# Performance work log

Hardware: AMD Instinct MI355X
Metric: run time of the kernel (lower is better)

## Reference

```python
import jax, jax.numpy as jnp
import numpy as np

H = 512        # HIDDEN_SIZE
HEADS = 4      # MEM_HEAD
KDIM = 256     # K_DIM (= H//2), HEADS*KDIM == 2*H
HALF = KDIM // 2
KNN = 32
SUB = 512      # SUB_SIZE
MEM = SUB * SUB
BN_EPS = 1e-5


def setup_inputs() -> dict:
    key = jax.random.key(0)
    ks = jax.random.split(key, 6)
    x = jax.random.normal(ks[0], (32, 64, H), jnp.float32)
    w1 = jax.random.normal(ks[1], (H // 2, H), jnp.float32) / np.sqrt(H).astype(np.float32)
    b1 = jnp.zeros((H // 2,), jnp.float32)
    w2 = jax.random.normal(ks[2], (2 * H, H // 2), jnp.float32) / np.sqrt(H // 2).astype(np.float32)
    b2 = jnp.zeros((2 * H,), jnp.float32)
    bn_gamma = jnp.ones((KDIM,), jnp.float32)
    bn_beta = jnp.zeros((KDIM,), jnp.float32)
    keys = jax.random.normal(ks[3], (HEADS, 2, SUB, HALF), jnp.float32) / np.sqrt(HALF).astype(np.float32)
    values = jax.random.normal(ks[4], (MEM, H), jnp.float32) * (H ** -0.5)
    return dict(x=x, w1=w1, b1=b1, w2=w2, b2=b2,
                bn_gamma=bn_gamma, bn_beta=bn_beta, keys=keys, values=values)


def reference(x, w1, b1, w2, b2, bn_gamma, bn_beta, keys, values):
    B, L, _ = x.shape
    n = B * L
    # Query MLP: H -> H/2 -> 2H, viewed as (n, HEADS, KDIM)
    h = jax.nn.relu(jnp.einsum('blh,ch->blc', x, w1) + b1)
    q = jnp.einsum('blc,dc->bld', h, w2) + b2                      # (B, L, 2H)
    q = q.reshape(n, HEADS, KDIM)
    # BatchNorm1d over the K_DIM channel (training-mode batch stats)
    flat = q.reshape(-1, KDIM)
    mean = flat.mean(0)
    var = flat.var(0)
    q = (q - mean) * jax.lax.rsqrt(var + BN_EPS) * bn_gamma + bn_beta
    # Product-key double top-k
    q1, q2 = q[..., :HALF], q[..., HALF:]
    s1 = jnp.einsum('nhd,hkd->nhk', q1, keys[:, 0])                # (n, HEADS, SUB)
    s2 = jnp.einsum('nhd,hkd->nhk', q2, keys[:, 1])
    ts1, ti1 = jax.lax.top_k(s1, KNN)
    ts2, ti2 = jax.lax.top_k(s2, KNN)
    all_s = (ts1[..., :, None] + ts2[..., None, :]).reshape(n, HEADS, KNN * KNN)
    all_i = (ti1[..., :, None] * SUB + ti2[..., None, :]).reshape(n, HEADS, KNN * KNN)
    sc, best = jax.lax.top_k(all_s, KNN)                            # (n, HEADS, KNN)
    idx = jnp.take_along_axis(all_i, best, axis=-1)
    # Softmax over KNN within each head (scores viewed as (-1, KNN))
    w = jax.nn.softmax(sc, axis=-1)
    idx = idx.reshape(n, HEADS * KNN)
    w = w.reshape(n, HEADS * KNN)
    # EmbeddingBag(mode='sum') with per-sample weights
    out = jnp.einsum('nkh,nk->nh', values[idx], w)                  # (n, H)
    out = out.reshape(B, L, H)
    return out.sum(1)                                               # (B, H)
```

## Files before the change

### kernel.cpp

```cpp
#include <hip/hip_runtime.h>
#include <hip/hip_bf16.h>
#include <math.h>

#define N_TOK   2048
#define HDIM    512
#define HHALF   256
#define QDIM    1024
#define KDIM    256
#define HALF    128
#define HEADS   4
#define KNN     32
#define SUB     512
#define NROWS   8192

__device__ __forceinline__ void gemm_tile_nt(
    const float* __restrict__ A, int lda,
    const float* __restrict__ B, int ldb,
    float* __restrict__ C, int ldc,
    int K, const float* __restrict__ bias, bool relu,
    int m0, int n0)
{
    __shared__ float As[16][68];
    __shared__ float Bs[16][68];
    int tid = threadIdx.x;
    int tx = tid & 15;
    int ty = tid >> 4;
    int lr = tid >> 2;
    int lc = (tid & 3) * 4;

    float acc[4][4] = {};

    for (int k0 = 0; k0 < K; k0 += 16) {
        float4 a = *(const float4*)(A + (size_t)(m0 + lr) * lda + k0 + lc);
        float4 b = *(const float4*)(B + (size_t)(n0 + lr) * ldb + k0 + lc);
        As[lc + 0][lr] = a.x; As[lc + 1][lr] = a.y;
        As[lc + 2][lr] = a.z; As[lc + 3][lr] = a.w;
        Bs[lc + 0][lr] = b.x; Bs[lc + 1][lr] = b.y;
        Bs[lc + 2][lr] = b.z; Bs[lc + 3][lr] = b.w;
        __syncthreads();
#pragma unroll
        for (int k = 0; k < 16; ++k) {
            float4 av = *(const float4*)&As[k][ty * 4];
            float4 bv = *(const float4*)&Bs[k][tx * 4];
            acc[0][0] = fmaf(av.x, bv.x, acc[0][0]);
            acc[0][1] = fmaf(av.x, bv.y, acc[0][1]);
            acc[0][2] = fmaf(av.x, bv.z, acc[0][2]);
            acc[0][3] = fmaf(av.x, bv.w, acc[0][3]);
            acc[1][0] = fmaf(av.y, bv.x, acc[1][0]);
            acc[1][1] = fmaf(av.y, bv.y, acc[1][1]);
            acc[1][2] = fmaf(av.y, bv.z, acc[1][2]);
            acc[1][3] = fmaf(av.y, bv.w, acc[1][3]);
            acc[2][0] = fmaf(av.z, bv.x, acc[2][0]);
            acc[2][1] = fmaf(av.z, bv.y, acc[2][1]);
            acc[2][2] = fmaf(av.z, bv.z, acc[2][2]);
            acc[2][3] = fmaf(av.z, bv.w, acc[2][3]);
            acc[3][0] = fmaf(av.w, bv.x, acc[3][0]);
            acc[3][1] = fmaf(av.w, bv.y, acc[3][1]);
            acc[3][2] = fmaf(av.w, bv.z, acc[3][2]);
            acc[3][3] = fmaf(av.w, bv.w, acc[3][3]);
        }
        __syncthreads();
    }

    float4 bb = make_float4(0.f, 0.f, 0.f, 0.f);
    if (bias) {
        bb.x = bias[n0 + tx * 4 + 0];
        bb.y = bias[n0 + tx * 4 + 1];
        bb.z = bias[n0 + tx * 4 + 2];
        bb.w = bias[n0 + tx * 4 + 3];
    }
#pragma unroll
    for (int i = 0; i < 4; ++i) {
        int m = m0 + ty * 4 + i;
        float4 r;
        r.x = acc[i][0] + bb.x;
        r.y = acc[i][1] + bb.y;
        r.z = acc[i][2] + bb.z;
        r.w = acc[i][3] + bb.w;
        if (relu) {
            r.x = fmaxf(r.x, 0.f); r.y = fmaxf(r.y, 0.f);
            r.z = fmaxf(r.z, 0.f); r.w = fmaxf(r.w, 0.f);
        }
        *(float4*)(C + (size_t)m * ldc + n0 + tx * 4) = r;
    }
}

__global__ __launch_bounds__(256) void gemm_nt_kernel(
    const float* __restrict__ A, int lda,
    const float* __restrict__ B, int ldb,
    float* __restrict__ C, int ldc,
    int K, const float* __restrict__ bias, int relu)
{
    gemm_tile_nt(A, lda, B, ldb, C, ldc, K, bias, relu != 0,
                 blockIdx.x * 64, blockIdx.y * 64);
}

__global__ __launch_bounds__(256) void score_kernel(
    const float* __restrict__ q, const float* __restrict__ keys,
    float* __restrict__ s1, float* __restrict__ s2)
{
    int z = blockIdx.z;
    int hh = z >> 1;
    int half = z & 1;
    const float* A = q + hh * KDIM + half * HALF;
    const float* B = keys + (size_t)z * SUB * HALF;
    float* C = (half ? s2 : s1) + hh * SUB;
    gemm_tile_nt(A, QDIM, B, HALF, C, HEADS * SUB, HALF, nullptr, false,
                 blockIdx.x * 64, blockIdx.y * 64);
}

__global__ __launch_bounds__(256) void bnstat_kernel(
    const float* __restrict__ q, float* __restrict__ partial)
{
    int c = threadIdx.x;
    int b = blockIdx.x;
    const float* base = q + (size_t)b * 32 * KDIM;
    float s = 0.f, s2 = 0.f;
#pragma unroll 8
    for (int r = 0; r < 32; ++r) {
        float v = base[r * KDIM + c];
        s += v;
        s2 = fmaf(v, v, s2);
    }
    partial[b * KDIM + c] = s;
    partial[256 * KDIM + b * KDIM + c] = s2;
}

__global__ __launch_bounds__(256) void bnfinal_kernel(
    const float* __restrict__ partial,
    const float* __restrict__ gamma, const float* __restrict__ beta,
    float* __restrict__ scsh)
{
    int c = threadIdx.x;
    float s = 0.f, s2 = 0.f;
    for (int b = 0; b < 256; ++b) {
        s += partial[b * KDIM + c];
        s2 += partial[256 * KDIM + b * KDIM + c];
    }
    float mean = s * (1.f / (float)NROWS);
    float var = s2 * (1.f / (float)NROWS) - mean * mean;
    float rstd = rsqrtf(var + 1e-5f);
    float sc = rstd * gamma[c];
    scsh[c] = sc;
    scsh[KDIM + c] = beta[c] - mean * sc;
}

__global__ __launch_bounds__(256) void bnapply_kernel(
    float* __restrict__ q, const float* __restrict__ scsh)
{
    int c = threadIdx.x;
    float sc = scsh[c];
    float sh = scsh[KDIM + c];
    size_t base = (size_t)blockIdx.x * 1024 + c;
#pragma unroll
    for (int r = 0; r < 4; ++r) {
        float v = q[base + r * KDIM];
        q[base + r * KDIM] = fmaf(v, sc, sh);
    }
}

__device__ __forceinline__ unsigned fmap(float f) {
    unsigned u = __float_as_uint(f);
    return (u & 0x80000000u) ? ~u : (u | 0x80000000u);
}

__device__ __forceinline__ int mbcnt64(unsigned long long m) {
    return __builtin_amdgcn_mbcnt_hi((unsigned)(m >> 32),
           __builtin_amdgcn_mbcnt_lo((unsigned)(m & 0xffffffffu), 0));
}

__global__ __launch_bounds__(256) void topk_kernel(
    const float* __restrict__ s1, const float* __restrict__ s2,
    int* __restrict__ out_idx, float* __restrict__ out_w)
{
    int w = threadIdx.x >> 6;
    int lane = threadIdx.x & 63;
    int task = blockIdx.x * 4 + w;

    __shared__ float ts1[4][KNN]; __shared__ int ti1[4][KNN];
    __shared__ float ts2[4][KNN]; __shared__ int ti2[4][KNN];
    __shared__ float scv[4][KNN]; __shared__ int scp[4][KNN];

    for (int src = 0; src < 2; ++src) {
        const float* base = (src ? s2 : s1) + (size_t)task * SUB;
        float v[8]; unsigned u[8];
#pragma unroll
        for (int i = 0; i < 8; ++i) {
            v[i] = base[lane + 64 * i];
            u[i] = fmap(v[i]);
        }
        unsigned t = 0u;
        for (int bit = 31; bit >= 0; --bit) {
            unsigned cand = t | (1u << bit);
            int cnt = 0;
#pragma unroll
            for (int i = 0; i < 8; ++i)
                cnt += __popcll(__ballot(u[i] >= cand));
            if (cnt >= KNN) t = cand;
        }
        float* tsv = src ? ts2[w] : ts1[w];
        int*   tsi = src ? ti2[w] : ti1[w];
        int pbase = 0;
#pragma unroll
        for (int i = 0; i < 8; ++i) {
            unsigned long long m = __ballot(u[i] >= t);
            if (u[i] >= t) {
                int pos = pbase + mbcnt64(m);
                if (pos < KNN) { tsv[pos] = v[i]; tsi[pos] = lane + 64 * i; }
            }
            pbase += __popcll(m);
        }
    }
    __syncthreads();

    float cv[16]; unsigned cu[16];
#pragma unroll
    for (int i = 0; i < 16; ++i) {
        int p = lane + 64 * i;
        cv[i] = ts1[w][p >> 5] + ts2[w][p & 31];
        cu[i] = fmap(cv[i]);
    }
    unsigned t2 = 0u;
    for (int bit = 31; bit >= 0; --bit) {
        unsigned cand = t2 | (1u << bit);
        int cnt = 0;
#pragma unroll
        for (int i = 0; i < 16; ++i)
            cnt += __popcll(__ballot(cu[i] >= cand));
        if (cnt >= KNN) t2 = cand;
    }
    int pbase = 0;
#pragma unroll
    for (int i = 0; i < 16; ++i) {
        unsigned long long m = __ballot(cu[i] >= t2);
        if (cu[i] >= t2) {
            int pos = pbase + mbcnt64(m);
            if (pos < KNN) { scv[w][pos] = cv[i]; scp[w][pos] = lane + 64 * i; }
        }
        pbase += __popcll(m);
    }
    __syncthreads();

    float x = (lane < KNN) ? scv[w][lane] : -3.0e38f;
    float mx = x;
#pragma unroll
    for (int off = 32; off; off >>= 1) mx = fmaxf(mx, __shfl_xor(mx, off));
    float e = (lane < KNN) ? expf(x - mx) : 0.f;
    float ssum = e;
#pragma unroll
    for (int off = 32; off; off >>= 1) ssum += __shfl_xor(ssum, off);

    if (lane < KNN) {
        int p = scp[w][lane];
        int i = p >> 5, j = p & 31;
        int gidx = ti1[w][i] * SUB + ti2[w][j];
        int n = task >> 2, h = task & 3;
        out_idx[n * (HEADS * KNN) + h * KNN + lane] = gidx;
        out_w[n * (HEADS * KNN) + h * KNN + lane] = e / ssum;
    }
}

__global__ __launch_bounds__(256) void gather_kernel(
    const float* __restrict__ values, const int* __restrict__ idx,
    const float* __restrict__ w, float* __restrict__ rows)
{
    int n = blockIdx.x;
    int tid = threadIdx.x;
    int pair = tid >> 7;
    int c4 = tid & 127;
    __shared__ int sidx[HEADS * KNN];
    __shared__ float sw[HEADS * KNN];
    __shared__ float4 tmp[128];
    if (tid < HEADS * KNN) {
        sidx[tid] = idx[n * (HEADS * KNN) + tid];
        sw[tid] = w[n * (HEADS * KNN) + tid];
    }
    __syncthreads();
    const float4* vv = (const float4*)values;
    float4 acc = make_float4(0.f, 0.f, 0.f, 0.f);
#pragma unroll 8
    for (int k = pair; k < HEADS * KNN; k += 2) {
        float4 v = vv[(size_t)sidx[k] * (HDIM / 4) + c4];
        float wk = sw[k];
        acc.x = fmaf(wk, v.x, acc.x);
        acc.y = fmaf(wk, v.y, acc.y);
        acc.z = fmaf(wk, v.z, acc.z);
        acc.w = fmaf(wk, v.w, acc.w);
    }
    if (pair) tmp[c4] = acc;
    __syncthreads();
    if (!pair) {
        float4 o = tmp[c4];
        acc.x += o.x; acc.y += o.y; acc.z += o.z; acc.w += o.w;
        ((float4*)rows)[(size_t)n * (HDIM / 4) + c4] = acc;
    }
}

__global__ __launch_bounds__(512) void reduce_kernel(
    const float* __restrict__ rows, float* __restrict__ out)
{
    int b = blockIdx.x;
    int c = threadIdx.x;
    float s = 0.f;
    for (int l = 0; l < 64; ++l)
        s += rows[(size_t)(b * 64 + l) * HDIM + c];
    out[b * HDIM + c] = s;
}

extern "C" void kernel_launch(void* const* d_in, const int* in_sizes, int n_in,
                              void* d_out, int out_size, void* d_ws, size_t ws_size,
                              hipStream_t stream)
{
    const float* x      = (const float*)d_in[0];
    const float* w1     = (const float*)d_in[1];
    const float* b1     = (const float*)d_in[2];
    const float* w2     = (const float*)d_in[3];
    const float* b2     = (const float*)d_in[4];
    const float* gamma  = (const float*)d_in[5];
    const float* beta   = (const float*)d_in[6];
    const float* keys   = (const float*)d_in[7];
    const float* values = (const float*)d_in[8];
    float* out = (float*)d_out;

    float* ws = (float*)d_ws;
    float* h       = ws;
    float* q       = h + N_TOK * HHALF;
    float* partial = q + N_TOK * QDIM;
    float* scsh    = partial + 2 * 256 * KDIM;
    float* s1      = scsh + 2 * KDIM;
    float* s2      = s1 + (size_t)N_TOK * HEADS * SUB;
    int*   tidx    = (int*)(s2 + (size_t)N_TOK * HEADS * SUB);
    float* tw      = (float*)(tidx + N_TOK * HEADS * KNN);
    float* rows    = tw + N_TOK * HEADS * KNN;

    gemm_nt_kernel<<<dim3(N_TOK / 64, HHALF / 64), 256, 0, stream>>>(
        x, HDIM, w1, HDIM, h, HHALF, HDIM, b1, 1);

    gemm_nt_kernel<<<dim3(N_TOK / 64, QDIM / 64), 256, 0, stream>>>(
        h, HHALF, w2, HHALF, q, QDIM, HHALF, b2, 0);

    bnstat_kernel<<<256, 256, 0, stream>>>(q, partial);
    bnfinal_kernel<<<1, 256, 0, stream>>>(partial, gamma, beta, scsh);
    bnapply_kernel<<<N_TOK, 256, 0, stream>>>(q, scsh);

    score_kernel<<<dim3(N_TOK / 64, SUB / 64, HEADS * 2), 256, 0, stream>>>(
        q, keys, s1, s2);

    topk_kernel<<<N_TOK * HEADS / 4, 256, 0, stream>>>(s1, s2, tidx, tw);

    gather_kernel<<<N_TOK, 256, 0, stream>>>(values, tidx, tw, rows);

    reduce_kernel<<<32, 512, 0, stream>>>(rows, out);
}
```

Baseline: 796.5 us.

## Fuse BN stats into fc2 GEMM, fold BN into keys, enlarge score tiles

Batch-norm statistics are now accumulated in the epilogue of the second MLP GEMM, which removes the separate stats pass over q. The normalization is no longer applied to q; it is folded algebraically into the product keys (keys scaled per channel, shift turned into a per-key bias), which removes the apply pass. The score GEMM moves to 128x128 tiles with 8x8 register blocking for more reuse. The top-k radix threshold search also exits early once exactly KNN candidates remain. The trade-off is higher register pressure in the score kernel and slightly different float rounding from the folded normalization.

After: 772.9 us. 3.0% less time.

```diff
diff --git a/kernel.cpp b/kernel.cpp
--- a/kernel.cpp
+++ b/kernel.cpp
@@ -95,47 +95,108 @@
                  blockIdx.x * 64, blockIdx.y * 64);
 }
 
-__global__ __launch_bounds__(256) void score_kernel(
-    const float* __restrict__ q, const float* __restrict__ keys,
-    float* __restrict__ s1, float* __restrict__ s2)
-{
-    int z = blockIdx.z;
-    int hh = z >> 1;
-    int half = z & 1;
-    const float* A = q + hh * KDIM + half * HALF;
-    const float* B = keys + (size_t)z * SUB * HALF;
-    float* C = (half ? s2 : s1) + hh * SUB;
-    gemm_tile_nt(A, QDIM, B, HALF, C, HEADS * SUB, HALF, nullptr, false,
-                 blockIdx.x * 64, blockIdx.y * 64);
-}
-
-__global__ __launch_bounds__(256) void bnstat_kernel(
-    const float* __restrict__ q, float* __restrict__ partial)
-{
-    int c = threadIdx.x;
-    int b = blockIdx.x;
-    const float* base = q + (size_t)b * 32 * KDIM;
-    float s = 0.f, s2 = 0.f;
-#pragma unroll 8
-    for (int r = 0; r < 32; ++r) {
-        float v = base[r * KDIM + c];
-        s += v;
-        s2 = fmaf(v, v, s2);
-    }
-    partial[b * KDIM + c] = s;
-    partial[256 * KDIM + b * KDIM + c] = s2;
+__global__ __launch_bounds__(256) void fc2_stats_kernel(
+    const float* __restrict__ A,
+    const float* __restrict__ B,
+    float* __restrict__ C,
+    const float* __restrict__ bias,
+    float* __restrict__ pstat)
+{
+    __shared__ float As[16][68];
+    __shared__ float Bs[16][68];
+    int tid = threadIdx.x;
+    int tx = tid & 15;
+    int ty = tid >> 4;
+    int lr = tid >> 2;
+    int lc = (tid & 3) * 4;
+    int m0 = blockIdx.x * 64;
+    int n0 = blockIdx.y * 64;
+
+    float acc[4][4] = {};
+
+    for (int k0 = 0; k0 < HHALF; k0 += 16) {
+        float4 a = *(const float4*)(A + (size_t)(m0 + lr) * HHALF + k0 + lc);
+        float4 b = *(const float4*)(B + (size_t)(n0 + lr) * HHALF + k0 + lc);
+        As[lc + 0][lr] = a.x; As[lc + 1][lr] = a.y;
+        As[lc + 2][lr] = a.z; As[lc + 3][lr] = a.w;
+        Bs[lc + 0][lr] = b.x; Bs[lc + 1][lr] = b.y;
+        Bs[lc + 2][lr] = b.z; Bs[lc + 3][lr] = b.w;
+        __syncthreads();
+#pragma unroll
+        for (int k = 0; k < 16; ++k) {
+            float4 av = *(const float4*)&As[k][ty * 4];
+            float4 bv = *(const float4*)&Bs[k][tx * 4];
+            acc[0][0] = fmaf(av.x, bv.x, acc[0][0]);
+            acc[0][1] = fmaf(av.x, bv.y, acc[0][1]);
+            acc[0][2] = fmaf(av.x, bv.z, acc[0][2]);
+            acc[0][3] = fmaf(av.x, bv.w, acc[0][3]);
+            acc[1][0] = fmaf(av.y, bv.x, acc[1][0]);
+            acc[1][1] = fmaf(av.y, bv.y, acc[1][1]);
+            acc[1][2] = fmaf(av.y, bv.z, acc[1][2]);
+            acc[1][3] = fmaf(av.y, bv.w, acc[1][3]);
+            acc[2][0] = fmaf(av.z, bv.x, acc[2][0]);
+            acc[2][1] = fmaf(av.z, bv.y, acc[2][1]);
+            acc[2][2] = fmaf(av.z, bv.z, acc[2][2]);
+            acc[2][3] = fmaf(av.z, bv.w, acc[2][3]);
+            acc[3][0] = fmaf(av.w, bv.x, acc[3][0]);
+            acc[3][1] = fmaf(av.w, bv.y, acc[3][1]);
+            acc[3][2] = fmaf(av.w, bv.z, acc[3][2]);
+            acc[3][3] = fmaf(av.w, bv.w, acc[3][3]);
+        }
+        __syncthreads();
+    }
+
+    float4 bb;
+    bb.x = bias[n0 + tx * 4 + 0];
+    bb.y = bias[n0 + tx * 4 + 1];
+    bb.z = bias[n0 + tx * 4 + 2];
+    bb.w = bias[n0 + tx * 4 + 3];
+    float4 cs  = make_float4(0.f, 0.f, 0.f, 0.f);
+    float4 csq = make_float4(0.f, 0.f, 0.f, 0.f);
+#pragma unroll
+    for (int i = 0; i < 4; ++i) {
+        int m = m0 + ty * 4 + i;
+        float4 r;
+        r.x = acc[i][0] + bb.x;
+        r.y = acc[i][1] + bb.y;
+        r.z = acc[i][2] + bb.z;
+        r.w = acc[i][3] + bb.w;
+        *(float4*)(C + (size_t)m * QDIM + n0 + tx * 4) = r;
+        cs.x += r.x; cs.y += r.y; cs.z += r.z; cs.w += r.w;
+        csq.x = fmaf(r.x, r.x, csq.x);
+        csq.y = fmaf(r.y, r.y, csq.y);
+        csq.z = fmaf(r.z, r.z, csq.z);
+        csq.w = fmaf(r.w, r.w, csq.w);
+    }
+    __syncthreads();
+    As[ty][tx * 4 + 0] = cs.x;  As[ty][tx * 4 + 1] = cs.y;
+    As[ty][tx * 4 + 2] = cs.z;  As[ty][tx * 4 + 3] = cs.w;
+    Bs[ty][tx * 4 + 0] = csq.x; Bs[ty][tx * 4 + 1] = csq.y;
+    Bs[ty][tx * 4 + 2] = csq.z; Bs[ty][tx * 4 + 3] = csq.w;
+    __syncthreads();
+    if (tid < 64) {
+        float s = 0.f, s2 = 0.f;
+#pragma unroll
+        for (int t = 0; t < 16; ++t) { s += As[t][tid]; s2 += Bs[t][tid]; }
+        int mb = blockIdx.x;
+        pstat[mb * QDIM + n0 + tid] = s;
+        pstat[32 * QDIM + mb * QDIM + n0 + tid] = s2;
+    }
 }
 
 __global__ __launch_bounds__(256) void bnfinal_kernel(
-    const float* __restrict__ partial,
+    const float* __restrict__ pstat,
     const float* __restrict__ gamma, const float* __restrict__ beta,
     float* __restrict__ scsh)
 {
     int c = threadIdx.x;
     float s = 0.f, s2 = 0.f;
-    for (int b = 0; b < 256; ++b) {
-        s += partial[b * KDIM + c];
-        s2 += partial[256 * KDIM + b * KDIM + c];
+    for (int mb = 0; mb < 32; ++mb) {
+#pragma unroll
+        for (int hd = 0; hd < 4; ++hd) {
+            s  += pstat[mb * QDIM + hd * KDIM + c];
+            s2 += pstat[32 * QDIM + mb * QDIM + hd * KDIM + c];
+        }
     }
     float mean = s * (1.f / (float)NROWS);
     float var = s2 * (1.f / (float)NROWS) - mean * mean;
@@ -145,17 +206,105 @@
     scsh[KDIM + c] = beta[c] - mean * sc;
 }
 
-__global__ __launch_bounds__(256) void bnapply_kernel(
-    float* __restrict__ q, const float* __restrict__ scsh)
-{
-    int c = threadIdx.x;
-    float sc = scsh[c];
-    float sh = scsh[KDIM + c];
-    size_t base = (size_t)blockIdx.x * 1024 + c;
-#pragma unroll
-    for (int r = 0; r < 4; ++r) {
-        float v = q[base + r * KDIM];
-        q[base + r * KDIM] = fmaf(v, sc, sh);
+__global__ __launch_bounds__(256) void prep_keys_kernel(
+    const float* __restrict__ keys, const float* __restrict__ scsh,
+    float* __restrict__ keys2, float* __restrict__ bias2)
+{
+    int z = blockIdx.x;
+    int kg = blockIdx.y;
+    int half = z & 1;
+    int tid = threadIdx.x;
+    int r = kg * 64 + (tid >> 2);
+    int d0 = (tid & 3) * 32;
+    const float* src = keys  + ((size_t)z * SUB + r) * HALF + d0;
+    float*       dst = keys2 + ((size_t)z * SUB + r) * HALF + d0;
+    const float* sc = scsh + half * HALF + d0;
+    const float* sh = scsh + KDIM + half * HALF + d0;
+    float part = 0.f;
+#pragma unroll
+    for (int j = 0; j < 32; j += 4) {
+        float4 kv = *(const float4*)(src + j);
+        float4 scv = *(const float4*)(sc + j);
+        float4 shv = *(const float4*)(sh + j);
+        float4 o;
+        o.x = kv.x * scv.x; o.y = kv.y * scv.y;
+        o.z = kv.z * scv.z; o.w = kv.w * scv.w;
+        part += kv.x * shv.x + kv.y * shv.y + kv.z * shv.z + kv.w * shv.w;
+        *(float4*)(dst + j) = o;
+    }
+    part += __shfl_xor(part, 1);
+    part += __shfl_xor(part, 2);
+    if ((tid & 3) == 0) bias2[z * SUB + r] = part;
+}
+
+__global__ __launch_bounds__(256) void score128_kernel(
+    const float* __restrict__ q, const float* __restrict__ keys2,
+    const float* __restrict__ bias2,
+    float* __restrict__ s1, float* __restrict__ s2)
+{
+    int z = blockIdx.z;
+    int hh = z >> 1;
+    int half = z & 1;
+    const float* A = q + hh * KDIM + half * HALF;
+    const float* B = keys2 + (size_t)z * SUB * HALF;
+    float* C = (half ? s2 : s1) + hh * SUB;
+    int m0 = blockIdx.x * 128;
+    int n0 = blockIdx.y * 128;
+
+    __shared__ float As[16][132];
+    __shared__ float Bs[16][132];
+    int tid = threadIdx.x;
+    int tx = tid & 15;
+    int ty = tid >> 4;
+    int lr = tid >> 1;
+    int lc = (tid & 1) * 8;
+
+    float acc[8][8] = {};
+
+#pragma unroll 1
+    for (int k0 = 0; k0 < HALF; k0 += 16) {
+        float4 a0 = *(const float4*)(A + (size_t)(m0 + lr) * QDIM + k0 + lc);
+        float4 a1 = *(const float4*)(A + (size_t)(m0 + lr) * QDIM + k0 + lc + 4);
+        float4 b0 = *(const float4*)(B + (size_t)(n0 + lr) * HALF + k0 + lc);
+        float4 b1 = *(const float4*)(B + (size_t)(n0 + lr) * HALF + k0 + lc + 4);
+        As[lc + 0][lr] = a0.x; As[lc + 1][lr] = a0.y;
+        As[lc + 2][lr] = a0.z; As[lc + 3][lr] = a0.w;
+        As[lc + 4][lr] = a1.x; As[lc + 5][lr] = a1.y;
+        As[lc + 6][lr] = a1.z; As[lc + 7][lr] = a1.w;
+        Bs[lc + 0][lr] = b0.x; Bs[lc + 1][lr] = b0.y;
+        Bs[lc + 2][lr] = b0.z; Bs[lc + 3][lr] = b0.w;
+        Bs[lc + 4][lr] = b1.x; Bs[lc + 5][lr] = b1.y;
+        Bs[lc + 6][lr] = b1.z; Bs[lc + 7][lr] = b1.w;
+        __syncthreads();
+#pragma unroll
+        for (int k = 0; k < 16; ++k) {
+            float4 av0 = *(const float4*)&As[k][ty * 8];
+            float4 av1 = *(const float4*)&As[k][ty * 8 + 4];
+            float4 bv0 = *(const float4*)&Bs[k][tx * 8];
+            float4 bv1 = *(const float4*)&Bs[k][tx * 8 + 4];
+            float a8[8] = {av0.x, av0.y, av0.z, av0.w, av1.x, av1.y, av1.z, av1.w};
+            float b8[8] = {bv0.x, bv0.y, bv0.z, bv0.w, bv1.x, bv1.y, bv1.z, bv1.w};
+#pragma unroll
+            for (int i = 0; i < 8; ++i)
+#pragma unroll
+                for (int j = 0; j < 8; ++j)
+                    acc[i][j] = fmaf(a8[i], b8[j], acc[i][j]);
+        }
+        __syncthreads();
+    }
+
+    float4 sb0 = *(const float4*)(bias2 + z * SUB + n0 + tx * 8);
+    float4 sb1 = *(const float4*)(bias2 + z * SUB + n0 + tx * 8 + 4);
+#pragma unroll
+    for (int i = 0; i < 8; ++i) {
+        int m = m0 + ty * 8 + i;
+        float4 r0, r1;
+        r0.x = acc[i][0] + sb0.x; r0.y = acc[i][1] + sb0.y;
+        r0.z = acc[i][2] + sb0.z; r0.w = acc[i][3] + sb0.w;
+        r1.x = acc[i][4] + sb1.x; r1.y = acc[i][5] + sb1.y;
+        r1.z = acc[i][6] + sb1.z; r1.w = acc[i][7] + sb1.w;
+        *(float4*)(C + (size_t)m * (HEADS * SUB) + n0 + tx * 8) = r0;
+        *(float4*)(C + (size_t)m * (HEADS * SUB) + n0 + tx * 8 + 4) = r1;
     }
 }
 
@@ -196,7 +345,8 @@
 #pragma unroll
             for (int i = 0; i < 8; ++i)
                 cnt += __popcll(__ballot(u[i] >= cand));
-            if (cnt >= KNN) t = cand;
+            if (cnt == KNN) { t = cand; break; }
+            if (cnt > KNN) t = cand;
         }
         float* tsv = src ? ts2[w] : ts1[w];
         int*   tsi = src ? ti2[w] : ti1[w];
@@ -227,7 +377,8 @@
 #pragma unroll
         for (int i = 0; i < 16; ++i)
             cnt += __popcll(__ballot(cu[i] >= cand));
-        if (cnt >= KNN) t2 = cand;
+        if (cnt == KNN) { t2 = cand; break; }
+        if (cnt > KNN) t2 = cand;
     }
     int pbase = 0;
 #pragma unroll
@@ -323,28 +474,30 @@
     float* out = (float*)d_out;
 
     float* ws = (float*)d_ws;
-    float* h       = ws;
-    float* q       = h + N_TOK * HHALF;
-    float* partial = q + N_TOK * QDIM;
-    float* scsh    = partial + 2 * 256 * KDIM;
-    float* s1      = scsh + 2 * KDIM;
-    float* s2      = s1 + (size_t)N_TOK * HEADS * SUB;
-    int*   tidx    = (int*)(s2 + (size_t)N_TOK * HEADS * SUB);
-    float* tw      = (float*)(tidx + N_TOK * HEADS * KNN);
-    float* rows    = tw + N_TOK * HEADS * KNN;
+    float* h     = ws;
+    float* q     = h + N_TOK * HHALF;
+    float* pstat = q + N_TOK * QDIM;
+    float* scsh  = pstat + 2 * 32 * QDIM;
+    float* keys2 = scsh + 2 * KDIM;
+    float* bias2 = keys2 + 8 * SUB * HALF;
+    float* s1    = bias2 + 8 * SUB;
+    float* s2    = s1 + (size_t)N_TOK * HEADS * SUB;
+    int*   tidx  = (int*)(s2 + (size_t)N_TOK * HEADS * SUB);
+    float* tw    = (float*)(tidx + N_TOK * HEADS * KNN);
+    float* rows  = tw + N_TOK * HEADS * KNN;
 
     gemm_nt_kernel<<<dim3(N_TOK / 64, HHALF / 64), 256, 0, stream>>>(
         x, HDIM, w1, HDIM, h, HHALF, HDIM, b1, 1);
 
-    gemm_nt_kernel<<<dim3(N_TOK / 64, QDIM / 64), 256, 0, stream>>>(
-        h, HHALF, w2, HHALF, q, QDIM, HHALF, b2, 0);
-
-    bnstat_kernel<<<256, 256, 0, stream>>>(q, partial);
-    bnfinal_kernel<<<1, 256, 0, stream>>>(partial, gamma, beta, scsh);
-    bnapply_kernel<<<N_TOK, 256, 0, stream>>>(q, scsh);
-
-    score_kernel<<<dim3(N_TOK / 64, SUB / 64, HEADS * 2), 256, 0, stream>>>(
-        q, keys, s1, s2);
+    fc2_stats_kernel<<<dim3(N_TOK / 64, QDIM / 64), 256, 0, stream>>>(
+        h, w2, q, b2, pstat);
+
+    bnfinal_kernel<<<1, 256, 0, stream>>>(pstat, gamma, beta, scsh);
+
+    prep_keys_kernel<<<dim3(8, 8), 256, 0, stream>>>(keys, scsh, keys2, bias2);
+
+    score128_kernel<<<dim3(N_TOK / 128, SUB / 128, HEADS * 2), 256, 0, stream>>>(
+        q, keys2, bias2, s1, s2);
 
     topk_kernel<<<N_TOK * HEADS / 4, 256, 0, stream>>>(s1, s2, tidx, tw);
 
```
